# Performance work log

Hardware: AMD Instinct MI355X
Metric: run time of the kernel (lower is better)

## Reference

```python
import jax, jax.numpy as jnp
import numpy as np

H_PARAM = 0.1  # bandwidth h
EPS_NORM = 1e-10
EPS_MIN = 0.001


def setup_inputs() -> dict:
    key = jax.random.key(0)
    k1, k2 = jax.random.split(key)
    feature_x = jax.random.normal(k1, (4, 64, 64, 128), dtype=jnp.float32)
    feature_y = jax.random.normal(k2, (4, 64, 64, 128), dtype=jnp.float32)
    return {"feature_x": feature_x, "feature_y": feature_y}


def reference(feature_x, feature_y):
    # NHWC -> NCHW
    fx = jnp.transpose(feature_x, (0, 3, 1, 2))
    fy = jnp.transpose(feature_y, (0, 3, 1, 2))
    B, C, H, W = fx.shape
    # center both features by spatial mean of feature_y (center_training=True, PONO=False)
    mean_y = jnp.mean(fy.reshape(B, C, -1), axis=-1)[:, :, None, None]  # [B,C,1,1]
    fx = fx - mean_y
    fy = fy - mean_y
    # flatten spatial, L2-normalize over channel dim
    fx = fx.reshape(B, C, -1)  # [B,C,N]
    fy = fy.reshape(B, C, -1)
    fx = fx / (jnp.linalg.norm(fx, ord=2, axis=1, keepdims=True) + EPS_NORM)
    fy = fy / (jnp.linalg.norm(fy, ord=2, axis=1, keepdims=True) + EPS_NORM)
    # cosine distance matrix d[b,n,m] = 1 - <fx[:, :, n], fy[:, :, m]>
    d = 1.0 - jnp.einsum('bcn,bcm->bnm', fx, fy)  # [B,N,N]
    # relative distance normalization
    d_norm = d / (jnp.min(d, axis=-1, keepdims=True) + EPS_MIN)
    # softmax-like affinity
    w = jnp.exp((1.0 - d_norm) / H_PARAM)
    A = w / jnp.sum(w, axis=-1, keepdims=True)
    # contextual similarity and loss
    CX = jnp.mean(jnp.max(A, axis=-1), axis=1)  # [B]
    return -jnp.log(CX)
```

## Files before the change

kernel.cpp:

```cpp
#include <hip/hip_runtime.h>
#include <hip/hip_bf16.h>
#include <math.h>

#define Bb   4
#define Cc   128
#define Nn   4096
#define BN   (Bb * Nn)
#define NSLC 4
#define HP   0.1f
#define EPSN 1e-10f
#define EPSM 0.001f

typedef __attribute__((ext_vector_type(8))) short short8;
typedef __attribute__((ext_vector_type(4))) float f32x4;

#define OFF_MEAN 0
#define OFF_ACC  512
#define OFF_PMAX 1024
#define OFF_SSP  263168
#define OFF_FXN  525312
#define OFF_FYN  1573888

__device__ __forceinline__ void gload_lds16(const void* g, void* l)
{
    __builtin_amdgcn_global_load_lds(
        (const __attribute__((address_space(1))) unsigned int*)g,
        (__attribute__((address_space(3))) unsigned int*)l, 16, 0, 0);
}

__global__ void k_mean(const float* __restrict__ fy, float* __restrict__ mean)
{
    int b = blockIdx.x >> 5;
    int chunk = blockIdx.x & 31;
    int c = threadIdx.x;
    const float* p = fy + ((size_t)b * Nn + (size_t)chunk * 128) * Cc + c;
    float s = 0.f;
    for (int n = 0; n < 128; ++n) s += p[(size_t)n * Cc];
    atomicAdd(&mean[b * Cc + c], s);
}

__global__ void k_norm(const float* __restrict__ fx, const float* __restrict__ fy,
                       const float* __restrict__ mean,
                       __hip_bfloat16* __restrict__ fxn, __hip_bfloat16* __restrict__ fyn)
{
    int grp = (blockIdx.x * 256 + threadIdx.x) >> 5;
    int sub = threadIdx.x & 31;
    int b   = grp >> 12;

    const float4* px = (const float4*)(fx + (size_t)grp * Cc);
    const float4* py = (const float4*)(fy + (size_t)grp * Cc);
    const float4* mp = (const float4*)(mean + b * Cc);

    float4 m = mp[sub];
    m.x *= (1.f / Nn); m.y *= (1.f / Nn); m.z *= (1.f / Nn); m.w *= (1.f / Nn);
    float4 x = px[sub], y = py[sub];
    x.x -= m.x; x.y -= m.y; x.z -= m.z; x.w -= m.w;
    y.x -= m.x; y.y -= m.y; y.z -= m.z; y.w -= m.w;

    float sx = x.x * x.x + x.y * x.y + x.z * x.z + x.w * x.w;
    float sy = y.x * y.x + y.y * y.y + y.z * y.z + y.w * y.w;
    #pragma unroll
    for (int o = 16; o > 0; o >>= 1) {
        sx += __shfl_xor(sx, o);
        sy += __shfl_xor(sy, o);
    }
    float ix = 1.f / (sqrtf(sx) + EPSN);
    float iy = 1.f / (sqrtf(sy) + EPSN);

    union { ushort4 u; __hip_bfloat16 h[4]; } ox, oy;
    ox.h[0] = __float2bfloat16(x.x * ix); ox.h[1] = __float2bfloat16(x.y * ix);
    ox.h[2] = __float2bfloat16(x.z * ix); ox.h[3] = __float2bfloat16(x.w * ix);
    oy.h[0] = __float2bfloat16(y.x * iy); oy.h[1] = __float2bfloat16(y.y * iy);
    oy.h[2] = __float2bfloat16(y.z * iy); oy.h[3] = __float2bfloat16(y.w * iy);
    ((ushort4*)(fxn + (size_t)grp * Cc))[sub] = ox.u;
    ((ushort4*)(fyn + (size_t)grp * Cc))[sub] = oy.u;
}

template <int PASS>
__global__ __launch_bounds__(256, 2) void k_gemm(
    const ushort* __restrict__ fxn, const ushort* __restrict__ fyn,
    float* __restrict__ pmax, float* __restrict__ ssp)
{
    __shared__ __align__(16) char smem[2 * 128 * 128 * 2];
    ushort* sBb  = (ushort*)smem;
    float*  sred = (float*)smem;
    __shared__ float sctv[256];

    const int tid  = threadIdx.x;
    const int lane = tid & 63;
    const int w    = tid >> 6;

    const int bid  = blockIdx.x;
    const int xcd  = bid & 7;
    const int s_   = bid >> 3;
    const int pair = xcd * 2 + (s_ >> 5);
    const int b    = pair >> 2;
    const int my   = pair & 3;
    const int n0   = (s_ & 31) * 128;

    const ushort* gA = fxn + (size_t)b * Nn * Cc;
    const ushort* gB = fyn + (size_t)b * Nn * Cc;

    if (PASS == 2 && tid < 128) {
        int row = b * Nn + n0 + tid;
        float g = -1e30f;
        #pragma unroll
        for (int z = 0; z < NSLC; ++z) g = fmaxf(g, pmax[(size_t)z * BN + row]);
        float d = 1.f - g;
        float t = 1.f / (HP * (d + EPSM));
        ((float2*)sctv)[tid] = (float2){(d - 1.f) * t, t};
    }

    const int l15 = lane & 15, q = lane >> 4;
    const int wy = w >> 1, wx = w & 1;

#define STAGE(mrow, bufidx)                                                    \
    {                                                                          \
        const ushort* src = gB + (size_t)(mrow) * Cc;                          \
        ushort* dstb = sBb + (bufidx) * 16384;                                 \
        _Pragma("unroll")                                                      \
        for (int inst = 0; inst < 8; ++inst) {                                 \
            int L0 = w * 512 + inst * 64;                                      \
            int L  = L0 + lane;                                                \
            int r = L >> 4, s2 = L & 15;                                       \
            int c = s2 ^ (r & 15);                                             \
            gload_lds16(src + (size_t)r * Cc + c * 8, dstb + L0 * 8);          \
        }                                                                      \
    }

    short8 afr[4][4];
    #pragma unroll
    for (int kt = 0; kt < 4; ++kt)
        #pragma unroll
        for (int i = 0; i < 4; ++i)
            afr[kt][i] = *(const short8*)(
                gA + (size_t)(n0 + wy * 64 + i * 16 + l15) * Cc + kt * 32 + q * 8);

    STAGE((my * 8) * 128, 0);
    STAGE((my * 8 + 1) * 128, 1);
    asm volatile("s_waitcnt vmcnt(8) lgkmcnt(0)" ::: "memory");
    __builtin_amdgcn_s_barrier();
    __builtin_amdgcn_sched_barrier(0);

    f32x4 acc[4][4];
    #pragma unroll
    for (int i = 0; i < 4; ++i)
        #pragma unroll
        for (int j = 0; j < 4; ++j)
            acc[i][j] = (f32x4){0.f, 0.f, 0.f, 0.f};

    float vpart[4][4];
    #pragma unroll
    for (int i = 0; i < 4; ++i)
        #pragma unroll
        for (int r = 0; r < 4; ++r)
            vpart[i][r] = (PASS == 1) ? -1e30f : 0.f;

    #pragma unroll
    for (int mt = 0; mt < 8; ++mt) {
        const ushort* sBc = sBb + (mt & 1) * 16384;
        #pragma unroll
        for (int kt = 0; kt < 4; ++kt) {
            short8 bb[4];
            #pragma unroll
            for (int j = 0; j < 4; ++j)
                bb[j] = *(const short8*)&sBc[(wx * 64 + j * 16 + l15) * 128
                                             + ((kt * 4 + q) ^ l15) * 8];
            #pragma unroll
            for (int i = 0; i < 4; ++i) {
                acc[i][0] = __builtin_amdgcn_mfma_f32_16x16x32_bf16(afr[kt][i], bb[0], acc[i][0], 0, 0, 0);
                acc[i][1] = __builtin_amdgcn_mfma_f32_16x16x32_bf16(afr[kt][i], bb[1], acc[i][1], 0, 0, 0);
                acc[i][2] = __builtin_amdgcn_mfma_f32_16x16x32_bf16(afr[kt][i], bb[2], acc[i][2], 0, 0, 0);
                acc[i][3] = __builtin_amdgcn_mfma_f32_16x16x32_bf16(afr[kt][i], bb[3], acc[i][3], 0, 0, 0);
            }
        }

        #pragma unroll
        for (int i = 0; i < 4; ++i) {
            #pragma unroll
            for (int r = 0; r < 4; ++r) {
                if (PASS == 1) {
                    float v = fmaxf(fmaxf(acc[i][0][r], acc[i][1][r]),
                                    fmaxf(acc[i][2][r], acc[i][3][r]));
                    vpart[i][r] = fmaxf(vpart[i][r], v);
                } else {
                    int row = wy * 64 + i * 16 + q * 4 + r;
                    float2 cc = ((const float2*)sctv)[row];
                    vpart[i][r] += __expf(fmaf(acc[i][0][r], cc.y, cc.x))
                                 + __expf(fmaf(acc[i][1][r], cc.y, cc.x))
                                 + __expf(fmaf(acc[i][2][r], cc.y, cc.x))
                                 + __expf(fmaf(acc[i][3][r], cc.y, cc.x));
                }
            }
            #pragma unroll
            for (int j = 0; j < 4; ++j)
                acc[i][j] = (f32x4){0.f, 0.f, 0.f, 0.f};
        }

        __builtin_amdgcn_sched_barrier(0);
        __builtin_amdgcn_s_barrier();
        __builtin_amdgcn_sched_barrier(0);
        if (mt < 6) STAGE((my * 8 + mt + 2) * 128, mt & 1);
        if (mt < 7) {
            if (mt < 6) { asm volatile("s_waitcnt vmcnt(8)" ::: "memory"); }
            else        { asm volatile("s_waitcnt vmcnt(0)" ::: "memory"); }
            __builtin_amdgcn_s_barrier();
            __builtin_amdgcn_sched_barrier(0);
        }
    }

#undef STAGE

    #pragma unroll
    for (int i = 0; i < 4; ++i)
        #pragma unroll
        for (int r = 0; r < 4; ++r) {
            int row = wy * 64 + i * 16 + q * 4 + r;
            sred[row * 36 + wx * 16 + l15] = vpart[i][r];
        }
    __syncthreads();
    if (tid < 128) {
        const float4* p = (const float4*)&sred[tid * 36];
        float4 v0 = p[0], v1 = p[1], v2 = p[2], v3 = p[3];
        float4 v4 = p[4], v5 = p[5], v6 = p[6], v7 = p[7];
        float v;
        if (PASS == 1) {
            float4 m01 = (float4){fmaxf(v0.x, v1.x), fmaxf(v0.y, v1.y),
                                  fmaxf(v0.z, v1.z), fmaxf(v0.w, v1.w)};
            float4 m23 = (float4){fmaxf(v2.x, v3.x), fmaxf(v2.y, v3.y),
                                  fmaxf(v2.z, v3.z), fmaxf(v2.w, v3.w)};
            float4 m45 = (float4){fmaxf(v4.x, v5.x), fmaxf(v4.y, v5.y),
                                  fmaxf(v4.z, v5.z), fmaxf(v4.w, v5.w)};
            float4 m67 = (float4){fmaxf(v6.x, v7.x), fmaxf(v6.y, v7.y),
                                  fmaxf(v6.z, v7.z), fmaxf(v6.w, v7.w)};
            float4 ma = (float4){fmaxf(m01.x, m23.x), fmaxf(m01.y, m23.y),
                                 fmaxf(m01.z, m23.z), fmaxf(m01.w, m23.w)};
            float4 mb = (float4){fmaxf(m45.x, m67.x), fmaxf(m45.y, m67.y),
                                 fmaxf(m45.z, m67.z), fmaxf(m45.w, m67.w)};
            v = fmaxf(fmaxf(fmaxf(ma.x, mb.x), fmaxf(ma.y, mb.y)),
                      fmaxf(fmaxf(ma.z, mb.z), fmaxf(ma.w, mb.w)));
        } else {
            float4 s01 = (float4){v0.x + v1.x, v0.y + v1.y,
                                  v0.z + v1.z, v0.w + v1.w};
            float4 s23 = (float4){v2.x + v3.x, v2.y + v3.y,
                                  v2.z + v3.z, v2.w + v3.w};
            float4 s45 = (float4){v4.x + v5.x, v4.y + v5.y,
                                  v4.z + v5.z, v4.w + v5.w};
            float4 s67 = (float4){v6.x + v7.x, v6.y + v7.y,
                                  v6.z + v7.z, v6.w + v7.w};
            v = (s01.x + s23.x) + (s01.y + s23.y)
              + (s01.z + s23.z) + (s01.w + s23.w)
              + (s45.x + s67.x) + (s45.y + s67.y)
              + (s45.z + s67.z) + (s45.w + s67.w);
        }
        float* dst = (PASS == 1) ? pmax : ssp;
        dst[(size_t)my * BN + b * Nn + n0 + tid] = v;
    }
}

__global__ void k_partial(const float* __restrict__ ssp, float* __restrict__ acc)
{
    int i = blockIdx.x * 256 + threadIdx.x;
    float t = 0.f;
    #pragma unroll
    for (int z = 0; z < NSLC; ++z) t += ssp[(size_t)z * BN + i];
    float s = 1.f / t;
    #pragma unroll
    for (int o = 32; o > 0; o >>= 1) s += __shfl_xor(s, o);
    __shared__ float red[4];
    if ((threadIdx.x & 63) == 0) red[threadIdx.x >> 6] = s;
    __syncthreads();
    if (threadIdx.x == 0)
        atomicAdd(&acc[i >> 12], red[0] + red[1] + red[2] + red[3]);
}

__global__ void k_out(const float* __restrict__ acc, float* __restrict__ out)
{
    int b = threadIdx.x;
    if (b < Bb) out[b] = -logf(acc[b] * (1.f / Nn));
}

extern "C" void kernel_launch(void* const* d_in, const int* in_sizes, int n_in,
                              void* d_out, int out_size, void* d_ws, size_t ws_size,
                              hipStream_t stream)
{
    const float* fx = (const float*)d_in[0];
    const float* fy = (const float*)d_in[1];
    float* out = (float*)d_out;
    float* ws  = (float*)d_ws;

    float* mean = ws + OFF_MEAN;
    float* acc  = ws + OFF_ACC;
    float* pmax = ws + OFF_PMAX;
    float* ssp  = ws + OFF_SSP;
    __hip_bfloat16* fxn = (__hip_bfloat16*)(ws + OFF_FXN);
    __hip_bfloat16* fyn = (__hip_bfloat16*)(ws + OFF_FYN);

    hipMemsetAsync(ws, 0, 516 * sizeof(float), stream);

    k_mean<<<dim3(Bb * 32), dim3(128), 0, stream>>>(fy, mean);
    k_norm<<<dim3(BN / 8), dim3(256), 0, stream>>>(fx, fy, mean, fxn, fyn);

    dim3 gg(512);
    k_gemm<1><<<gg, dim3(256), 0, stream>>>((const ushort*)fxn, (const ushort*)fyn,
                                            pmax, nullptr);
    k_gemm<2><<<gg, dim3(256), 0, stream>>>((const ushort*)fxn, (const ushort*)fyn,
                                            pmax, ssp);
    k_partial<<<dim3(BN / 256), dim3(256), 0, stream>>>(ssp, acc);
    k_out<<<dim3(1), dim3(64), 0, stream>>>(acc, out);
}
```

Before: 117.0 us.

## Overlap epilogue with next tile prefetch, fold log2e, cache row constants in registers

Moves the per-tile max/exp-sum epilogue after the barrier and the async load of the next B tile, so the epilogue math overlaps the global-to-LDS prefetch. Folds log2(e) into the per-row scale so exp2f replaces __expf. Hoists the row constants from LDS into registers once per block, and seeds the first MFMA with a zero accumulator instead of zeroing the accumulators explicitly. Keeping the row constants in registers for the whole loop raises register pressure, which may lower occupancy.

```diff
diff --git a/kernel.cpp b/kernel.cpp
--- a/kernel.cpp
+++ b/kernel.cpp
@@ -107,7 +107,7 @@
         #pragma unroll
         for (int z = 0; z < NSLC; ++z) g = fmaxf(g, pmax[(size_t)z * BN + row]);
         float d = 1.f - g;
-        float t = 1.f / (HP * (d + EPSM));
+        float t = (1.4426950408889634f / HP) / (d + EPSM);
         ((float2*)sctv)[tid] = (float2){(d - 1.f) * t, t};
     }
 
@@ -142,12 +142,16 @@
     __builtin_amdgcn_s_barrier();
     __builtin_amdgcn_sched_barrier(0);
 
-    f32x4 acc[4][4];
-    #pragma unroll
-    for (int i = 0; i < 4; ++i)
-        #pragma unroll
-        for (int j = 0; j < 4; ++j)
-            acc[i][j] = (f32x4){0.f, 0.f, 0.f, 0.f};
+    float2 ccr[4][4];
+    if (PASS == 2) {
+        #pragma unroll
+        for (int i = 0; i < 4; ++i)
+            #pragma unroll
+            for (int r = 0; r < 4; ++r)
+                ccr[i][r] = ((const float2*)sctv)[wy * 64 + i * 16 + q * 4 + r];
+    }
+
+    const f32x4 zacc = (f32x4){0.f, 0.f, 0.f, 0.f};
 
     float vpart[4][4];
     #pragma unroll
@@ -159,6 +163,7 @@
     #pragma unroll
     for (int mt = 0; mt < 8; ++mt) {
         const ushort* sBc = sBb + (mt & 1) * 16384;
+        f32x4 acc[4][4];
         #pragma unroll
         for (int kt = 0; kt < 4; ++kt) {
             short8 bb[4];
@@ -167,41 +172,38 @@
                 bb[j] = *(const short8*)&sBc[(wx * 64 + j * 16 + l15) * 128
                                              + ((kt * 4 + q) ^ l15) * 8];
             #pragma unroll
-            for (int i = 0; i < 4; ++i) {
-                acc[i][0] = __builtin_amdgcn_mfma_f32_16x16x32_bf16(afr[kt][i], bb[0], acc[i][0], 0, 0, 0);
-                acc[i][1] = __builtin_amdgcn_mfma_f32_16x16x32_bf16(afr[kt][i], bb[1], acc[i][1], 0, 0, 0);
-                acc[i][2] = __builtin_amdgcn_mfma_f32_16x16x32_bf16(afr[kt][i], bb[2], acc[i][2], 0, 0, 0);
-                acc[i][3] = __builtin_amdgcn_mfma_f32_16x16x32_bf16(afr[kt][i], bb[3], acc[i][3], 0, 0, 0);
-            }
-        }
-
-        #pragma unroll
-        for (int i = 0; i < 4; ++i) {
-            #pragma unroll
-            for (int r = 0; r < 4; ++r) {
-                if (PASS == 1) {
-                    float v = fmaxf(fmaxf(acc[i][0][r], acc[i][1][r]),
-                                    fmaxf(acc[i][2][r], acc[i][3][r]));
-                    vpart[i][r] = fmaxf(vpart[i][r], v);
-                } else {
-                    int row = wy * 64 + i * 16 + q * 4 + r;
-                    float2 cc = ((const float2*)sctv)[row];
-                    vpart[i][r] += __expf(fmaf(acc[i][0][r], cc.y, cc.x))
-                                 + __expf(fmaf(acc[i][1][r], cc.y, cc.x))
-                                 + __expf(fmaf(acc[i][2][r], cc.y, cc.x))
-                                 + __expf(fmaf(acc[i][3][r], cc.y, cc.x));
-                }
-            }
-            #pragma unroll
-            for (int j = 0; j < 4; ++j)
-                acc[i][j] = (f32x4){0.f, 0.f, 0.f, 0.f};
+            for (int i = 0; i < 4; ++i)
+                #pragma unroll
+                for (int j = 0; j < 4; ++j)
+                    acc[i][j] = __builtin_amdgcn_mfma_f32_16x16x32_bf16(
+                        afr[kt][i], bb[j],
+                        (kt == 0) ? zacc : acc[i][j], 0, 0, 0);
         }
 
         __builtin_amdgcn_sched_barrier(0);
         __builtin_amdgcn_s_barrier();
         __builtin_amdgcn_sched_barrier(0);
         if (mt < 6) STAGE((my * 8 + mt + 2) * 128, mt & 1);
+
+        #pragma unroll
+        for (int i = 0; i < 4; ++i)
+            #pragma unroll
+            for (int r = 0; r < 4; ++r) {
+                if (PASS == 1) {
+                    vpart[i][r] = fmaxf(vpart[i][r],
+                        fmaxf(fmaxf(acc[i][0][r], acc[i][1][r]),
+                              fmaxf(acc[i][2][r], acc[i][3][r])));
+                } else {
+                    float2 cc = ccr[i][r];
+                    vpart[i][r] += exp2f(fmaf(acc[i][0][r], cc.y, cc.x))
+                                 + exp2f(fmaf(acc[i][1][r], cc.y, cc.x))
+                                 + exp2f(fmaf(acc[i][2][r], cc.y, cc.x))
+                                 + exp2f(fmaf(acc[i][3][r], cc.y, cc.x));
+                }
+            }
+
         if (mt < 7) {
+            __builtin_amdgcn_sched_barrier(0);
             if (mt < 6) { asm volatile("s_waitcnt vmcnt(8)" ::: "memory"); }
             else        { asm volatile("s_waitcnt vmcnt(0)" ::: "memory"); }
             __builtin_amdgcn_s_barrier();
```

After: 128.4 us. 1.1x slower.
